# Optimization experiments

Hardware: AMD Instinct MI355X
Metric: run time of the kernel (lower is better)

The kernel has to match this reference:

```python
import jax, jax.numpy as jnp
import numpy as np

N_NODES = 2048
N_EDGES = 32768
N_IN = 256
MSG_HID = 512
MSG_OUT = 256
N_HID = 512


def _linear_params(key, fan_in, fan_out):
    kw, kb = jax.random.split(key)
    bound = 1.0 / np.sqrt(fan_in)
    W = jax.random.uniform(kw, (fan_out, fan_in), jnp.float32, -bound, bound)
    b = jax.random.uniform(kb, (fan_out,), jnp.float32, -bound, bound)
    return W, b


def setup_inputs() -> dict:
    key = jax.random.key(0)
    ks = jax.random.split(key, 8)
    inputs = jax.random.normal(ks[0], (N_NODES, N_IN), jnp.float32)
    # one-hot incidence matrices built from random receiver/sender node indices
    recv_idx = jax.random.randint(ks[1], (N_EDGES,), 0, N_NODES)
    send_idx = jax.random.randint(ks[2], (N_EDGES,), 0, N_NODES)
    rel_rec = jax.nn.one_hot(recv_idx, N_NODES, dtype=jnp.float32)   # [E, N]
    rel_send = jax.nn.one_hot(send_idx, N_NODES, dtype=jnp.float32)  # [E, N]
    msg_W1, msg_b1 = _linear_params(ks[3], 2 * N_IN, MSG_HID)
    msg_W2, msg_b2 = _linear_params(ks[4], MSG_HID, MSG_OUT)
    out_W1, out_b1 = _linear_params(ks[5], N_IN + MSG_OUT, N_HID)
    out_W2, out_b2 = _linear_params(ks[6], N_HID, N_HID)
    out_W3, out_b3 = _linear_params(ks[7], N_HID, N_IN)
    return {
        'inputs': inputs, 'rel_rec': rel_rec, 'rel_send': rel_send,
        'msg_W1': msg_W1, 'msg_b1': msg_b1, 'msg_W2': msg_W2, 'msg_b2': msg_b2,
        'out_W1': out_W1, 'out_b1': out_b1, 'out_W2': out_W2, 'out_b2': out_b2,
        'out_W3': out_W3, 'out_b3': out_b3,
    }


def reference(inputs, rel_rec, rel_send, msg_W1, msg_b1, msg_W2, msg_b2,
              out_W1, out_b1, out_W2, out_b2, out_W3, out_b3):
    # gather node features to edges via dense one-hot matmuls (as in original)
    receivers = rel_rec @ inputs    # [E, n_in]
    senders = rel_send @ inputs     # [E, n_in]
    pre_msg = jnp.concatenate([senders, receivers], axis=1)  # [E, 2*n_in]
    # edge-message MLP (dropout p=0 -> identity)
    msg = jax.nn.relu(pre_msg @ msg_W1.T + msg_b1)
    msg = jax.nn.relu(msg @ msg_W2.T + msg_b2)               # [E, msg_out]
    # scatter-add messages to receiving nodes: (msg^T @ rel_rec)^T == rel_rec^T @ msg
    agg_msgs = rel_rec.T @ msg                               # [N, msg_out]
    aug_inputs = jnp.concatenate([inputs, agg_msgs], axis=-1)
    # node-update MLP
    pred = jax.nn.relu(aug_inputs @ out_W1.T + out_b1)
    pred = jax.nn.relu(pred @ out_W2.T + out_b2)
    pred = pred @ out_W3.T + out_b3
    return inputs + pred
```

## Files before the change

### kernel.cpp

```cpp
#include <hip/hip_runtime.h>
#include <hip/hip_bf16.h>
#include <stdint.h>

using bf16 = __hip_bfloat16;
typedef short bf16x8 __attribute__((ext_vector_type(8)));
typedef float floatx4 __attribute__((ext_vector_type(4)));

static constexpr int NODES = 2048;
static constexpr int EDGES = 32768;

__device__ inline uint4 cvt8(const float* __restrict__ p) {
    const float4* f = (const float4*)p;
    float4 a = f[0], b = f[1];
    union { uint4 u; bf16 h[8]; } pk;
    pk.h[0] = __float2bfloat16(a.x); pk.h[1] = __float2bfloat16(a.y);
    pk.h[2] = __float2bfloat16(a.z); pk.h[3] = __float2bfloat16(a.w);
    pk.h[4] = __float2bfloat16(b.x); pk.h[5] = __float2bfloat16(b.y);
    pk.h[6] = __float2bfloat16(b.z); pk.h[7] = __float2bfloat16(b.w);
    return pk.u;
}

template<int BM, int BN, int AMODE, int BMODE, int EPI>
__device__ __forceinline__ void gemm_body(
    const bf16* __restrict__ A, const float* __restrict__ Af,
    const float* __restrict__ Bt, const float* __restrict__ bias,
    bf16* __restrict__ Cout, float* __restrict__ OutF,
    const float* __restrict__ inputsF, const bf16* __restrict__ UVb,
    const float* __restrict__ b1v, const int* __restrict__ sidx,
    const int* __restrict__ ridx, const float* __restrict__ aggin,
    float* __restrict__ aggout, int M, int N, int K, int bx, int by)
{
    constexpr int BK = 32;
    constexpr int PA = BM / 64;
    constexpr int PB = BN / 64;
    constexpr int MI = BM / 32;
    constexpr int NJ = BN / 32;
    __shared__ bf16 As[BM * BK];
    __shared__ bf16 Bs[BN * BK];
    __shared__ int sIdx[BM];
    __shared__ int rIdx[BM];

    const int t = threadIdx.x;
    const int m0 = by * BM;
    const int n0 = bx * BN;

    if constexpr (AMODE == 3) {
        if (t < BM) {
            sIdx[t] = sidx[m0 + t] & (NODES - 1);
            rIdx[t] = ridx[m0 + t] & (NODES - 1);
        }
        __syncthreads();
    }

    const int sr = t >> 2;
    const int sc = t & 3;

    uint4 ra[PA], rb[PB];

    auto loadTiles = [&](int kt) {
        const int kk = kt * BK + sc * 8;
#pragma unroll
        for (int p = 0; p < PA; ++p) {
            const int row = p * 64 + sr;
            if constexpr (AMODE == 0) {
                ra[p] = *(const uint4*)(A + (size_t)(m0 + row) * K + kk);
            } else if constexpr (AMODE == 1) {
                ra[p] = cvt8(Af + (size_t)(m0 + row) * K + kk);
            } else if constexpr (AMODE == 2) {
                const float* src = (kk < 256)
                    ? (inputsF + (size_t)(m0 + row) * 256 + kk)
                    : (aggin + (size_t)(m0 + row) * 256 + (kk - 256));
                ra[p] = cvt8(src);
            } else {
                union { uint4 q; unsigned short h[8]; } uu, vv;
                uu.q = *(const uint4*)(UVb + (size_t)sIdx[row] * 1024 + kk);
                vv.q = *(const uint4*)(UVb + (size_t)rIdx[row] * 1024 + 512 + kk);
                const float4* c = (const float4*)(b1v + kk);
                float4 c0 = c[0], c1 = c[1];
                const float cf[8] = {c0.x, c0.y, c0.z, c0.w, c1.x, c1.y, c1.z, c1.w};
                union { uint4 q; bf16 h[8]; } pk;
#pragma unroll
                for (int e = 0; e < 8; ++e) {
                    union { unsigned int u; float f; } a2, b2;
                    a2.u = (unsigned int)uu.h[e] << 16;
                    b2.u = (unsigned int)vv.h[e] << 16;
                    pk.h[e] = __float2bfloat16(fmaxf(a2.f + b2.f + cf[e], 0.f));
                }
                ra[p] = pk.q;
            }
        }
#pragma unroll
        for (int p = 0; p < PB; ++p) {
            const int row = p * 64 + sr;
            if constexpr (BMODE == 0) {
                rb[p] = cvt8(Bt + (size_t)(n0 + row) * K + kk);
            } else {
                const int n = n0 + row;
                rb[p] = cvt8(Bt + (size_t)(n & 511) * 512 + (n >> 9) * 256 + kk);
            }
        }
    };

    const int wv = t >> 6;
    const int lane = t & 63;
    const int wm = wv >> 1, wn = wv & 1;
    const int r16 = lane & 15, q = lane >> 4;

    floatx4 acc[MI][NJ] = {};

    loadTiles(0);
    const int KT = K / BK;
    for (int kt = 0; kt < KT; ++kt) {
        __syncthreads();
#pragma unroll
        for (int p = 0; p < PA; ++p)
            *(uint4*)(&As[(p * 64 + sr) * BK + sc * 8]) = ra[p];
#pragma unroll
        for (int p = 0; p < PB; ++p)
            *(uint4*)(&Bs[(p * 64 + sr) * BK + sc * 8]) = rb[p];
        __syncthreads();
        if (kt + 1 < KT) loadTiles(kt + 1);

        bf16x8 af[MI], bfr[NJ];
#pragma unroll
        for (int i = 0; i < MI; ++i)
            af[i] = *(const bf16x8*)(&As[(wm * (BM / 2) + i * 16 + r16) * BK + q * 8]);
#pragma unroll
        for (int j = 0; j < NJ; ++j)
            bfr[j] = *(const bf16x8*)(&Bs[(wn * (BN / 2) + j * 16 + r16) * BK + q * 8]);
#pragma unroll
        for (int i = 0; i < MI; ++i)
#pragma unroll
            for (int j = 0; j < NJ; ++j)
                acc[i][j] = __builtin_amdgcn_mfma_f32_16x16x32_bf16(af[i], bfr[j], acc[i][j], 0, 0, 0);
    }

    float bv[NJ];
#pragma unroll
    for (int j = 0; j < NJ; ++j)
        bv[j] = (EPI == 3 || EPI == 4) ? 0.f : bias[n0 + wn * (BN / 2) + j * 16 + r16];

#pragma unroll
    for (int i = 0; i < MI; ++i) {
        const int lr = wm * (BM / 2) + i * 16 + q * 4;
        const int rbase = m0 + lr;
#pragma unroll
        for (int j = 0; j < NJ; ++j) {
            const int gc = n0 + wn * (BN / 2) + j * 16 + r16;
#pragma unroll
            for (int r = 0; r < 4; ++r) {
                float v = acc[i][j][r] + bv[j];
                const int gr = rbase + r;
                if constexpr (EPI == 0) {
                    v = fmaxf(v, 0.0f);
                    Cout[(size_t)gr * N + gc] = __float2bfloat16(v);
                } else if constexpr (EPI == 1) {
                    v = fmaxf(v, 0.0f);
                    atomicAdd(&aggout[(size_t)rIdx[lr + r] * 256 + gc], v);
                } else if constexpr (EPI == 2) {
                    OutF[(size_t)gr * 256 + gc] = inputsF[(size_t)gr * 256 + gc] + v;
                } else if constexpr (EPI == 3) {
                    OutF[(size_t)gr * N + gc] = v;
                } else {
                    Cout[(size_t)gr * N + gc] = __float2bfloat16(v);
                }
            }
        }
    }
}

template<int BM, int BN, int AMODE, int BMODE, int EPI>
__global__ __launch_bounds__(256, 2) void gemm_k(
    const bf16* __restrict__ A, const float* __restrict__ Af,
    const float* __restrict__ Bt, const float* __restrict__ bias,
    bf16* __restrict__ Cout, float* __restrict__ OutF,
    const float* __restrict__ inputsF, const bf16* __restrict__ UVb,
    const float* __restrict__ b1v, const int* __restrict__ sidx,
    const int* __restrict__ ridx, const float* __restrict__ aggin,
    float* __restrict__ aggout, int M, int N, int K)
{
    gemm_body<BM, BN, AMODE, BMODE, EPI>(A, Af, Bt, bias, Cout, OutF, inputsF,
        UVb, b1v, sidx, ridx, aggin, aggout, M, N, K, blockIdx.x, blockIdx.y);
}

__global__ __launch_bounds__(256, 8) void fat_pre(
    const float* __restrict__ rel_rec, const float* __restrict__ rel_send,
    int* __restrict__ recv_idx, int* __restrict__ send_idx,
    float4* __restrict__ agg, const float* __restrict__ inputs,
    const float* __restrict__ msg_W1, bf16* __restrict__ UVb)
{
    const int b = blockIdx.x;
    if (b < 512) {
        gemm_body<64, 64, 1, 1, 4>(nullptr, inputs, msg_W1, nullptr, UVb, nullptr,
            nullptr, nullptr, nullptr, nullptr, nullptr, nullptr, nullptr,
            NODES, 1024, 256, b & 15, b >> 4);
    } else if (b < 1024) {
        agg[(size_t)(b - 512) * 256 + threadIdx.x] = float4{0.f, 0.f, 0.f, 0.f};
    } else {
        const int eb = b - 1024;
        const int half = eb >> 13;
        const int rb = eb & 8191;
        const float* mat = half ? rel_send : rel_rec;
        int* out = half ? send_idx : recv_idx;
        const int w = threadIdx.x >> 6;
        const int lane = threadIdx.x & 63;
        const int row = rb * 4 + w;
        if (lane == 0) out[row] = 0;
        const uint4* base = (const uint4*)(mat + (size_t)row * NODES);
        for (int p = 0; p < 8; ++p) {
            uint4 v = base[p * 64 + lane];
            const bool hit = (v.x | v.y | v.z | v.w) != 0u;
            if (hit) {
                int e = v.x ? 0 : (v.y ? 1 : (v.z ? 2 : 3));
                out[row] = p * 256 + lane * 4 + e;
            }
            if (__any(hit)) break;
        }
    }
}

extern "C" void kernel_launch(void* const* d_in, const int* in_sizes, int n_in,
                              void* d_out, int out_size, void* d_ws, size_t ws_size,
                              hipStream_t stream) {
    const float* inputs   = (const float*)d_in[0];
    const float* rel_rec  = (const float*)d_in[1];
    const float* rel_send = (const float*)d_in[2];
    const float* msg_W1   = (const float*)d_in[3];
    const float* msg_b1   = (const float*)d_in[4];
    const float* msg_W2   = (const float*)d_in[5];
    const float* msg_b2   = (const float*)d_in[6];
    const float* out_W1   = (const float*)d_in[7];
    const float* out_b1   = (const float*)d_in[8];
    const float* out_W2   = (const float*)d_in[9];
    const float* out_b2   = (const float*)d_in[10];
    const float* out_W3   = (const float*)d_in[11];
    const float* out_b3   = (const float*)d_in[12];

    char* ws = (char*)d_ws;
    int*   recv_idx = (int*)(ws + 0);
    int*   send_idx = (int*)(ws + 131072);
    float* agg      = (float*)(ws + 262144);
    bf16*  UVb      = (bf16*)(ws + 2359296);
    bf16*  g1       = (bf16*)(ws + 6553600);
    bf16*  g2       = (bf16*)(ws + 8650752);
    if (ws_size < (size_t)11 * 1024 * 1024) return;

    fat_pre<<<17408, 256, 0, stream>>>(rel_rec, rel_send, recv_idx, send_idx,
                                       (float4*)agg, inputs, msg_W1, UVb);

    gemm_k<128, 128, 3, 0, 1><<<dim3(2, 256), 256, 0, stream>>>(
        nullptr, nullptr, msg_W2, msg_b2, nullptr, nullptr,
        nullptr, UVb, msg_b1, send_idx, recv_idx, nullptr, agg,
        EDGES, 256, 512);

    gemm_k<64, 64, 2, 0, 0><<<dim3(8, 32), 256, 0, stream>>>(
        nullptr, nullptr, out_W1, out_b1, g1, nullptr,
        inputs, nullptr, nullptr, nullptr, nullptr, agg, nullptr,
        NODES, 512, 512);

    gemm_k<64, 64, 0, 0, 0><<<dim3(8, 32), 256, 0, stream>>>(
        g1, nullptr, out_W2, out_b2, g2, nullptr,
        nullptr, nullptr, nullptr, nullptr, nullptr, nullptr, nullptr,
        NODES, 512, 512);

    gemm_k<64, 64, 0, 0, 2><<<dim3(4, 32), 256, 0, stream>>>(
        g2, nullptr, out_W3, out_b3, nullptr, (float*)d_out,
        inputs, nullptr, nullptr, nullptr, nullptr, nullptr, nullptr,
        NODES, 256, 512);
}
```

Measured before the change: 595.3 us.

## Fuse node-update MLP into one kernel and pre-convert weights to bf16

Replaces the three separate node-MLP GEMM launches with one fused kernel. Each 16-row block keeps its activations in shared memory across all three layers, and each wave reads its weight fragments directly from global memory. The fp32 weights for msg_W2 and the three output layers are converted to bf16 once in the preprocessing kernel, so the edge GEMM loads bf16 weights directly. This removes two launches and the g1/g2 round trips, but only 128 blocks run the node MLP and each block re-reads all weights from global memory or cache.

```diff
diff --git a/kernel.cpp b/kernel.cpp
--- a/kernel.cpp
+++ b/kernel.cpp
@@ -94,6 +94,8 @@
             const int row = p * 64 + sr;
             if constexpr (BMODE == 0) {
                 rb[p] = cvt8(Bt + (size_t)(n0 + row) * K + kk);
+            } else if constexpr (BMODE == 2) {
+                rb[p] = *(const uint4*)(((const bf16*)Bt) + (size_t)(n0 + row) * K + kk);
             } else {
                 const int n = n0 + row;
                 rb[p] = cvt8(Bt + (size_t)(n & 511) * 512 + (n >> 9) * 256 + kk);
@@ -183,11 +185,101 @@
         UVb, b1v, sidx, ridx, aggin, aggout, M, N, K, blockIdx.x, blockIdx.y);
 }
 
+template<int NJ, int EPI>
+__device__ __forceinline__ void mlp_layer(
+    const bf16* __restrict__ Asrc, const bf16* __restrict__ W,
+    const float* __restrict__ bias, bf16* __restrict__ dst,
+    const float* __restrict__ inputsF, float* __restrict__ outF,
+    int m0, int wv, int r16, int q)
+{
+    constexpr int LDR = 520;
+    const int ncol0 = wv * NJ * 16;
+    floatx4 acc[NJ] = {};
+    bf16x8 bb0[NJ], bb1[NJ];
+    bf16x8 aa0, aa1;
+
+    auto loadB = [&](int kt, bf16x8* d) {
+#pragma unroll
+        for (int j = 0; j < NJ; ++j)
+            d[j] = *(const bf16x8*)(W + (size_t)(ncol0 + j * 16 + r16) * 512 + kt * 32 + q * 8);
+    };
+    auto loadA = [&](int kt) {
+        return *(const bf16x8*)(Asrc + r16 * LDR + kt * 32 + q * 8);
+    };
+
+    loadB(0, bb0); aa0 = loadA(0);
+#pragma unroll
+    for (int kt = 0; kt < 16; kt += 2) {
+        loadB(kt + 1, bb1); aa1 = loadA(kt + 1);
+#pragma unroll
+        for (int j = 0; j < NJ; ++j)
+            acc[j] = __builtin_amdgcn_mfma_f32_16x16x32_bf16(aa0, bb0[j], acc[j], 0, 0, 0);
+        if (kt + 2 < 16) { loadB(kt + 2, bb0); aa0 = loadA(kt + 2); }
+#pragma unroll
+        for (int j = 0; j < NJ; ++j)
+            acc[j] = __builtin_amdgcn_mfma_f32_16x16x32_bf16(aa1, bb1[j], acc[j], 0, 0, 0);
+    }
+
+#pragma unroll
+    for (int j = 0; j < NJ; ++j) {
+        const int gc = ncol0 + j * 16 + r16;
+        const float bvv = bias[gc];
+#pragma unroll
+        for (int r = 0; r < 4; ++r) {
+            float v = acc[j][r] + bvv;
+            const int lr = q * 4 + r;
+            if constexpr (EPI == 0) {
+                dst[lr * LDR + gc] = __float2bfloat16(fmaxf(v, 0.f));
+            } else {
+                const size_t o = (size_t)(m0 + lr) * 256 + gc;
+                outF[o] = inputsF[o] + v;
+            }
+        }
+    }
+}
+
+__global__ __launch_bounds__(256, 2) void node_mlp(
+    const float* __restrict__ inputs, const float* __restrict__ agg,
+    const bf16* __restrict__ W1b, const float* __restrict__ b1,
+    const bf16* __restrict__ W2b, const float* __restrict__ b2,
+    const bf16* __restrict__ W3b, const float* __restrict__ b3,
+    float* __restrict__ out)
+{
+    constexpr int LDR = 520;
+    __shared__ bf16 As[16 * LDR];
+    __shared__ bf16 Hs[16 * LDR];
+    __shared__ bf16 Gs[16 * LDR];
+    const int t = threadIdx.x;
+    const int m0 = blockIdx.x * 16;
+
+#pragma unroll
+    for (int p = 0; p < 4; ++p) {
+        const int c = t + 256 * p;
+        const int row = c >> 6;
+        const int col = (c & 63) * 8;
+        const float* src = (col < 256)
+            ? (inputs + (size_t)(m0 + row) * 256 + col)
+            : (agg + (size_t)(m0 + row) * 256 + (col - 256));
+        *(uint4*)(&As[row * LDR + col]) = cvt8(src);
+    }
+    const int wv = t >> 6, lane = t & 63;
+    const int r16 = lane & 15, q = lane >> 4;
+    __syncthreads();
+    mlp_layer<8, 0>(As, W1b, b1, Hs, nullptr, nullptr, m0, wv, r16, q);
+    __syncthreads();
+    mlp_layer<8, 0>(Hs, W2b, b2, Gs, nullptr, nullptr, m0, wv, r16, q);
+    __syncthreads();
+    mlp_layer<4, 1>(Gs, W3b, b3, nullptr, inputs, out, m0, wv, r16, q);
+}
+
 __global__ __launch_bounds__(256, 8) void fat_pre(
     const float* __restrict__ rel_rec, const float* __restrict__ rel_send,
     int* __restrict__ recv_idx, int* __restrict__ send_idx,
     float4* __restrict__ agg, const float* __restrict__ inputs,
-    const float* __restrict__ msg_W1, bf16* __restrict__ UVb)
+    const float* __restrict__ msg_W1, bf16* __restrict__ UVb,
+    const float* __restrict__ msg_W2, const float* __restrict__ out_W1,
+    const float* __restrict__ out_W2, const float* __restrict__ out_W3,
+    bf16* __restrict__ Wc)
 {
     const int b = blockIdx.x;
     if (b < 512) {
@@ -196,8 +288,16 @@
             NODES, 1024, 256, b & 15, b >> 4);
     } else if (b < 1024) {
         agg[(size_t)(b - 512) * 256 + threadIdx.x] = float4{0.f, 0.f, 0.f, 0.f};
+    } else if (b < 1408) {
+        const int gid = (b - 1024) * 2048 + threadIdx.x * 8;
+        const float* src;
+        if (gid < 131072)      src = msg_W2 + gid;
+        else if (gid < 393216) src = out_W1 + (gid - 131072);
+        else if (gid < 655360) src = out_W2 + (gid - 393216);
+        else                   src = out_W3 + (gid - 655360);
+        *(uint4*)(Wc + gid) = cvt8(src);
     } else {
-        const int eb = b - 1024;
+        const int eb = b - 1408;
         const int half = eb >> 13;
         const int rb = eb & 8191;
         const float* mat = half ? rel_send : rel_rec;
@@ -241,30 +341,22 @@
     int*   send_idx = (int*)(ws + 131072);
     float* agg      = (float*)(ws + 262144);
     bf16*  UVb      = (bf16*)(ws + 2359296);
-    bf16*  g1       = (bf16*)(ws + 6553600);
-    bf16*  g2       = (bf16*)(ws + 8650752);
+    bf16*  Wc       = (bf16*)(ws + 6553600);
+    bf16*  W2b  = Wc;
+    bf16*  oW1b = Wc + 131072;
+    bf16*  oW2b = Wc + 393216;
+    bf16*  oW3b = Wc + 655360;
     if (ws_size < (size_t)11 * 1024 * 1024) return;
 
-    fat_pre<<<17408, 256, 0, stream>>>(rel_rec, rel_send, recv_idx, send_idx,
-                                       (float4*)agg, inputs, msg_W1, UVb);
-
-    gemm_k<128, 128, 3, 0, 1><<<dim3(2, 256), 256, 0, stream>>>(
-        nullptr, nullptr, msg_W2, msg_b2, nullptr, nullptr,
+    fat_pre<<<17792, 256, 0, stream>>>(rel_rec, rel_send, recv_idx, send_idx,
+                                       (float4*)agg, inputs, msg_W1, UVb,
+                                       msg_W2, out_W1, out_W2, out_W3, Wc);
+
+    gemm_k<128, 128, 3, 2, 1><<<dim3(2, 256), 256, 0, stream>>>(
+        nullptr, nullptr, (const float*)W2b, msg_b2, nullptr, nullptr,
         nullptr, UVb, msg_b1, send_idx, recv_idx, nullptr, agg,
         EDGES, 256, 512);
 
-    gemm_k<64, 64, 2, 0, 0><<<dim3(8, 32), 256, 0, stream>>>(
-        nullptr, nullptr, out_W1, out_b1, g1, nullptr,
-        inputs, nullptr, nullptr, nullptr, nullptr, agg, nullptr,
-        NODES, 512, 512);
-
-    gemm_k<64, 64, 0, 0, 0><<<dim3(8, 32), 256, 0, stream>>>(
-        g1, nullptr, out_W2, out_b2, g2, nullptr,
-        nullptr, nullptr, nullptr, nullptr, nullptr, nullptr, nullptr,
-        NODES, 512, 512);
-
-    gemm_k<64, 64, 0, 0, 2><<<dim3(4, 32), 256, 0, stream>>>(
-        g2, nullptr, out_W3, out_b3, nullptr, (float*)d_out,
-        inputs, nullptr, nullptr, nullptr, nullptr, nullptr, nullptr,
-        NODES, 256, 512);
-}
+    node_mlp<<<128, 256, 0, stream>>>(
+        inputs, agg, oW1b, out_b1, oW2b, out_b2, oW3b, out_b3, (float*)d_out);
+}
```

New measurement: 584.3 us. Within noise of the previous version (-1.9%).
